# Optimization experiments

Measured on AMD Instinct MI355X. Metric: run time of the kernel, lower is better.

The kernel has to match this reference:

```python
import jax, jax.numpy as jnp
import numpy as np

N_FEAT = 1024
NEG_BIG = -1e30  # finite stand-in for -inf to avoid NaNs on fully-masked rows


def setup_inputs() -> dict:
    key = jax.random.key(0)
    k1, k2, k3 = jax.random.split(key, 3)
    T, C = 4096, 1024
    x = jax.random.normal(k1, (T, C), dtype=jnp.float32)
    W = jax.random.normal(k2, (C, 3 * N_FEAT), dtype=jnp.float32) * 0.02
    b = jax.random.normal(k3, (3 * N_FEAT,), dtype=jnp.float32) * 0.02
    return {"x": x, "W": W, "b": b, "n_padd": 256}


def reference(x, W, b, n_padd):
    T, C = x.shape
    qkv = x @ W + b  # [T, 3*N_FEAT]
    q, k, v = jnp.split(qkv, 3, axis=1)  # each [T, N_FEAT]
    att = (q @ k.T) * (1.0 / jnp.sqrt(jnp.float32(N_FEAT)))  # [T, T]
    idx = jnp.arange(T)
    causal = idx[None, :] <= idx[:, None]
    data = (idx[None, :] >= n_padd) & (idx[:, None] >= n_padd)
    mask = causal & data
    att = jnp.where(mask, att, NEG_BIG)
    p = jax.nn.softmax(att, axis=-1)  # fully-masked rows -> uniform, zeroed below
    y = p @ v  # [T, N_FEAT]
    # kernel only stores rows >= n_padd; padded rows defined as zero here
    y = jnp.where(idx[:, None] >= n_padd, y, 0.0)
    return y
```

## Files before the change

### kernel.cpp

```cpp
#include <hip/hip_runtime.h>
#include <hip/hip_bf16.h>
#include <stdint.h>
#include <stddef.h>

#define TT 4096
#define CC 1024
#define NFD 1024
#define N3 3072
#define PB0 1152
#define PB2 2176

typedef __bf16 bf16;
typedef __bf16 bf16x8 __attribute__((ext_vector_type(8)));
typedef __bf16 bf16x4 __attribute__((ext_vector_type(4)));
typedef float f32x4 __attribute__((ext_vector_type(4)));

typedef const __attribute__((address_space(1))) unsigned char gl_u8;
typedef __attribute__((address_space(3))) unsigned char lds_u8;

__device__ __forceinline__ void glds16(const void* g, void* l) {
  __builtin_amdgcn_global_load_lds((gl_u8*)g, (lds_u8*)l, 16, 0, 0);
}

__device__ __forceinline__ void stage128x32(const bf16* __restrict__ src, int ld, bf16* lds, int tid) {
  const int lane = tid & 63;
  const int w = tid >> 6;
#pragma unroll
  for (int p = 0; p < 2; ++p) {
    const int lbyte = w * 2048 + p * 1024;
    const int row = (lbyte >> 6) + (lane >> 2);
    const int kel = (lane & 3) << 3;
    glds16(src + row * ld + kel, (char*)lds + lbyte);
  }
}

__device__ __forceinline__ void gemm_core(const bf16* __restrict__ A, const bf16* __restrict__ B,
                                          int lda, int ldb, int ksteps,
                                          bf16* As, bf16* Bs, int tid, f32x4 (&acc)[4][4]) {
  const int lane = tid & 63;
  const int w = tid >> 6;
  const int wm = (w >> 1) * 64;
  const int wn = (w & 1) * 64;
  const int lrow = lane & 15;
  const int lko = (lane >> 4) * 8;
  stage128x32(A, lda, As, tid);
  stage128x32(B, ldb, Bs, tid);
  __syncthreads();
  for (int ks = 0; ks < ksteps; ++ks) {
    const bf16* Ac = As + (ks & 1) * 4096;
    const bf16* Bc = Bs + (ks & 1) * 4096;
    if (ks + 1 < ksteps) {
      stage128x32(A + (ks + 1) * 32, lda, As + ((ks + 1) & 1) * 4096, tid);
      stage128x32(B + (ks + 1) * 32, ldb, Bs + ((ks + 1) & 1) * 4096, tid);
    }
    bf16x8 af[4], bfr[4];
#pragma unroll
    for (int i = 0; i < 4; ++i)
      af[i] = *(const bf16x8*)(Ac + (wm + i * 16 + lrow) * 32 + lko);
#pragma unroll
    for (int i = 0; i < 4; ++i)
      bfr[i] = *(const bf16x8*)(Bc + (wn + i * 16 + lrow) * 32 + lko);
#pragma unroll
    for (int mi = 0; mi < 4; ++mi)
#pragma unroll
      for (int ni = 0; ni < 4; ++ni)
        acc[mi][ni] = __builtin_amdgcn_mfma_f32_16x16x32_bf16(af[mi], bfr[ni], acc[mi][ni], 0, 0, 0);
    __syncthreads();
  }
}

__global__ __launch_bounds__(256) void k_prep(const float* __restrict__ x, bf16* __restrict__ xb,
                                              const float* __restrict__ Wsrc, bf16* __restrict__ WbT,
                                              float* __restrict__ l) {
  __shared__ float Ls[64][68];
  const int tid = threadIdx.x;
  if (blockIdx.x < 2048) {
    int idx = (blockIdx.x * 256 + tid) * 8;
    f32x4 a = *(const f32x4*)(x + idx);
    f32x4 b = *(const f32x4*)(x + idx + 4);
    bf16x8 o;
#pragma unroll
    for (int j = 0; j < 4; ++j) { o[j] = (bf16)a[j]; o[4 + j] = (bf16)b[j]; }
    *(bf16x8*)(xb + idx) = o;
    return;
  }
  if (blockIdx.x == 2048 + 768) {
    f32x4 z = (f32x4){0.f, 0.f, 0.f, 0.f};
#pragma unroll
    for (int qq = 0; qq < 4; ++qq)
      *(f32x4*)(l + (qq * 256 + tid) * 4) = z;
    return;
  }
  const int bid = blockIdx.x - 2048;
  const int n0 = (bid % 48) * 64;
  const int c0 = (bid / 48) * 64;
#pragma unroll
  for (int qq = 0; qq < 4; ++qq) {
    int lin = qq * 1024 + tid * 4;
    int r = lin >> 6, cc = lin & 63;
    f32x4 v = *(const f32x4*)(Wsrc + (size_t)(c0 + r) * N3 + n0 + cc);
#pragma unroll
    for (int j = 0; j < 4; ++j) Ls[r][cc + j] = v[j];
  }
  __syncthreads();
#pragma unroll
  for (int qq = 0; qq < 4; ++qq) {
    int lin = qq * 1024 + tid * 4;
    int nr = lin >> 6, cc = lin & 63;
    bf16x4 o;
#pragma unroll
    for (int j = 0; j < 4; ++j) o[j] = (bf16)Ls[cc + j][nr];
    *(bf16x4*)(WbT + (size_t)(n0 + nr) * CC + c0 + cc) = o;
  }
}

__global__ __launch_bounds__(256, 2) void k_qkv(const bf16* __restrict__ xb, const bf16* __restrict__ wbt,
                                                const float* __restrict__ bias,
                                                bf16* __restrict__ q, bf16* __restrict__ k,
                                                bf16* __restrict__ vT) {
  __shared__ bf16 As[2 * 128 * 32], Bs[2 * 128 * 32];
  const int tid = threadIdx.x;
  const int id = blockIdx.x;
  const int r = id & 7;
  const int s = id >> 3;
  const int it = 4 * r + (s & 3);
  const int jt = s >> 2;
  const int m0 = it * 128;
  const int n0 = jt * 128;
  f32x4 acc[4][4];
#pragma unroll
  for (int i = 0; i < 4; ++i)
#pragma unroll
    for (int j = 0; j < 4; ++j) acc[i][j] = (f32x4){0.f, 0.f, 0.f, 0.f};

  gemm_core(xb + (size_t)m0 * CC, wbt + (size_t)n0 * CC, CC, CC, CC / 32, As, Bs, tid, acc);

  const int lane = tid & 63;
  const int w = tid >> 6;
  const int wm = (w >> 1) * 64, wn = (w & 1) * 64;
  const int seg = n0 >> 10;
#pragma unroll
  for (int mi = 0; mi < 4; ++mi) {
    const int tB = m0 + wm + mi * 16 + ((lane >> 4) << 2);
#pragma unroll
    for (int ni = 0; ni < 4; ++ni) {
      const int n = n0 + wn + ni * 16 + (lane & 15);
      const float bb = bias[n];
      f32x4 a = acc[mi][ni];
      if (seg == 2) {
        bf16x4 pv;
#pragma unroll
        for (int r2 = 0; r2 < 4; ++r2) pv[r2] = (bf16)(a[r2] + bb);
        *(bf16x4*)(vT + (size_t)(n - 2048) * TT + tB) = pv;
      } else {
        bf16* dst = (seg == 0) ? q : k;
        const int nl = n & 1023;
#pragma unroll
        for (int r2 = 0; r2 < 4; ++r2) dst[(size_t)(tB + r2) * NFD + nl] = (bf16)(a[r2] + bb);
      }
    }
  }
}

__global__ __launch_bounds__(256, 2) void k_scores(const bf16* __restrict__ q, const bf16* __restrict__ kk,
                                                   bf16* __restrict__ P, float* __restrict__ l,
                                                   const int* __restrict__ npadd_p) {
  const int id = blockIdx.x;
  const int lin = (id & 7) * 66 + (id >> 3);
  int band, rem;
  if (lin < 228)      { band = 0; rem = lin; }
  else if (lin < 392) { band = 1; rem = lin - 228; }
  else if (lin < 492) { band = 2; rem = lin - 392; }
  else                { band = 3; rem = lin - 492; }
  int it, jt;
  if (rem < 28) {
    int itp = (int)((sqrtf(8.0f * (float)rem + 1.0f) - 1.0f) * 0.5f);
    while ((itp + 1) * (itp + 2) / 2 <= rem) ++itp;
    while (itp * (itp + 1) / 2 > rem) --itp;
    it = band * 8 + itp;
    jt = band * 8 + (rem - itp * (itp + 1) / 2);
  } else {
    const int rem2 = rem - 28;
    it = band * 8 + 7 + (rem2 >> 3);
    jt = band * 8 + (rem2 & 7);
  }
  const int np = *npadd_p;
  const int jt0 = np >> 7;
  if (jt < jt0) return;

  __shared__ bf16 As[2 * 128 * 32], Bs[2 * 128 * 32];
  const int tid = threadIdx.x;
  f32x4 acc[4][4];
#pragma unroll
  for (int i = 0; i < 4; ++i)
#pragma unroll
    for (int j = 0; j < 4; ++j) acc[i][j] = (f32x4){0.f, 0.f, 0.f, 0.f};

  gemm_core(q + (size_t)it * 128 * CC, kk + (size_t)jt * 128 * CC, CC, CC, CC / 32, As, Bs, tid, acc);

  const int lane = tid & 63;
  const int w = tid >> 6;
  const int wm = (w >> 1) * 64, wn = (w & 1) * 64;
  const float scale = 0.03125f;
#pragma unroll
  for (int mi = 0; mi < 4; ++mi) {
    const int iB = it * 128 + wm + mi * 16 + ((lane >> 4) << 2);
    float rs[4] = {0.f, 0.f, 0.f, 0.f};
#pragma unroll
    for (int ni = 0; ni < 4; ++ni) {
      const int j = jt * 128 + wn + ni * 16 + (lane & 15);
      f32x4 a = acc[mi][ni];
#pragma unroll
      for (int r = 0; r < 4; ++r) {
        const int i = iB + r;
        float p = 0.f;
        if (j <= i && j >= np && i >= np) p = __expf(a[r] * scale);
        const bf16 pb = (bf16)p;
        P[(size_t)i * TT + j] = pb;
        rs[r] += (float)pb;
      }
    }
#pragma unroll
    for (int r = 0; r < 4; ++r) {
      float v = rs[r];
      v += __shfl_xor(v, 1);
      v += __shfl_xor(v, 2);
      v += __shfl_xor(v, 4);
      v += __shfl_xor(v, 8);
      if ((lane & 15) == 0) atomicAdd(&l[iB + r], v);
    }
  }
}

__global__ __launch_bounds__(256, 2) void k_pvc(const bf16* __restrict__ P, const bf16* __restrict__ vT,
                                                bf16* __restrict__ part0, bf16* __restrict__ part1,
                                                bf16* __restrict__ part2,
                                                const float* __restrict__ l, float* __restrict__ y,
                                                const int* __restrict__ npadd_p) {
  const int id = blockIdx.x;
  const int kgrp = id >> 3;
  const int d0 = (kgrp & 7) * 128;
  const int p = (id & 7) + 8 * (kgrp >> 3);
  const int it = p >> 2;
  const int c = p & 3;
  const int np = *npadd_p;
  const int jt0 = np >> 7;
  const int lo = (c == 0) ? 0 : (c == 1 ? 9 : (c == 2 ? 17 : 25));
  const int hi = (c == 0) ? 9 : (c == 1 ? 17 : (c == 2 ? 25 : 32));
  const int jlo = max(lo, jt0);
  const int jhi = min(hi, it + 1);
  if (jlo >= jhi) return;

  __shared__ bf16 As[2 * 128 * 32], Bs[2 * 128 * 32];
  const int tid = threadIdx.x;
  f32x4 acc[4][4];
#pragma unroll
  for (int i = 0; i < 4; ++i)
#pragma unroll
    for (int j = 0; j < 4; ++j) acc[i][j] = (f32x4){0.f, 0.f, 0.f, 0.f};

  gemm_core(P + (size_t)it * 128 * TT + (size_t)jlo * 128,
            vT + (size_t)d0 * TT + (size_t)jlo * 128,
            TT, TT, (jhi - jlo) * 4, As, Bs, tid, acc);

  const int lane = tid & 63;
  const int w = tid >> 6;
  const int wm = (w >> 1) * 64, wn = (w & 1) * 64;
  const bool sole = (jlo == jt0) && (jhi == it + 1);
  if (sole) {
#pragma unroll
    for (int mi = 0; mi < 4; ++mi) {
      const int iB = it * 128 + wm + mi * 16 + ((lane >> 4) << 2);
      float inv4[4];
#pragma unroll
      for (int r = 0; r < 4; ++r) {
        const int i = iB + r;
        inv4[r] = (i >= np) ? (1.0f / l[i]) : 0.0f;
      }
#pragma unroll
      for (int ni = 0; ni < 4; ++ni) {
        const int d = d0 + wn + ni * 16 + (lane & 15);
        f32x4 a = acc[mi][ni];
#pragma unroll
        for (int r = 0; r < 4; ++r)
          y[(size_t)(iB + r) * NFD + d] = a[r] * inv4[r];
      }
    }
  } else if (c == 3) {
#pragma unroll
    for (int mi = 0; mi < 4; ++mi) {
      const int iB = it * 128 + wm + mi * 16 + ((lane >> 4) << 2);
#pragma unroll
      for (int ni = 0; ni < 4; ++ni) {
        const int d = d0 + wn + ni * 16 + (lane & 15);
        f32x4 a = acc[mi][ni];
#pragma unroll
        for (int r = 0; r < 4; ++r)
          y[(size_t)(iB + r) * NFD + d] = a[r];
      }
    }
  } else {
    bf16* __restrict__ part = (c == 0) ? part0 : (c == 1 ? part1 : part2);
    const int base = (c == 2) ? (PB2 * NFD) : (PB0 * NFD);
#pragma unroll
    for (int mi = 0; mi < 4; ++mi) {
      const int iB = it * 128 + wm + mi * 16 + ((lane >> 4) << 2);
#pragma unroll
      for (int ni = 0; ni < 4; ++ni) {
        const int d = d0 + wn + ni * 16 + (lane & 15);
        f32x4 a = acc[mi][ni];
#pragma unroll
        for (int r = 0; r < 4; ++r)
          part[(size_t)(iB + r) * NFD + d - base] = (bf16)a[r];
      }
    }
  }
}

__global__ __launch_bounds__(256) void k_norm(const bf16* __restrict__ part0, const bf16* __restrict__ part1,
                                              const bf16* __restrict__ part2,
                                              const float* __restrict__ l, float* __restrict__ y,
                                              const int* __restrict__ npadd_p) {
  const int idx = (blockIdx.x * 256 + threadIdx.x) * 8;
  const int i = idx >> 10;
  const int np = *npadd_p;
  if (i < np) {
    f32x4 z = (f32x4){0.f, 0.f, 0.f, 0.f};
    *(f32x4*)(y + idx) = z;
    *(f32x4*)(y + idx + 4) = z;
    return;
  }
  const int jt0 = np >> 7;
  const int it = i >> 7;
  const int ip1 = it + 1;
  const bool a0 = (max(0, jt0)  < min(9, ip1));
  const bool a1 = (max(9, jt0)  < min(17, ip1));
  const bool a2 = (max(17, jt0) < min(25, ip1));
  const bool a3 = (max(25, jt0) < min(32, ip1));
  const int cnt = (int)a0 + (int)a1 + (int)a2 + (int)a3;
  if (cnt <= 1) return;
  float s[8] = {0.f, 0.f, 0.f, 0.f, 0.f, 0.f, 0.f, 0.f};
  if (a0) {
    bf16x8 a = *(const bf16x8*)(part0 + idx - PB0 * NFD);
#pragma unroll
    for (int j = 0; j < 8; ++j) s[j] += (float)a[j];
  }
  if (a1) {
    bf16x8 a = *(const bf16x8*)(part1 + idx - PB0 * NFD);
#pragma unroll
    for (int j = 0; j < 8; ++j) s[j] += (float)a[j];
  }
  if (a2) {
    bf16x8 a = *(const bf16x8*)(part2 + idx - PB2 * NFD);
#pragma unroll
    for (int j = 0; j < 8; ++j) s[j] += (float)a[j];
  }
  if (a3) {
    f32x4 a = *(const f32x4*)(y + idx);
    f32x4 b = *(const f32x4*)(y + idx + 4);
#pragma unroll
    for (int j = 0; j < 4; ++j) { s[j] += a[j]; s[4 + j] += b[j]; }
  }
  const float inv = 1.0f / l[i];
  f32x4 o0, o1;
#pragma unroll
  for (int j = 0; j < 4; ++j) { o0[j] = s[j] * inv; o1[j] = s[4 + j] * inv; }
  *(f32x4*)(y + idx) = o0;
  *(f32x4*)(y + idx + 4) = o1;
}

extern "C" void kernel_launch(void* const* d_in, const int* in_sizes, int n_in,
                              void* d_out, int out_size, void* d_ws, size_t ws_size,
                              hipStream_t stream) {
  const float* x = (const float*)d_in[0];
  const float* W = (const float*)d_in[1];
  const float* b = (const float*)d_in[2];
  const int* npadd = (const int*)d_in[3];
  float* y = (float*)d_out;

  char* ws = (char*)d_ws;
  const size_t MB = 1u << 20;
  bf16* q  = (bf16*)(ws + 0 * MB);
  bf16* kk = (bf16*)(ws + 8 * MB);
  bf16* part0 = (bf16*)(ws + 0 * MB);
  bf16* part1 = (bf16*)(ws + (size_t)(TT - PB0) * NFD * 2);
  bf16* part2 = (bf16*)(ws + (size_t)2 * (TT - PB0) * NFD * 2);
  bf16* vT = (bf16*)(ws + 16 * MB);
  float* l = (float*)(ws + 24 * MB);
  bf16* P  = (bf16*)(ws + 24 * MB + 65536);
  bf16* xb = P;
  bf16* WbT = (bf16*)((char*)P + 8 * MB);

  k_prep<<<dim3(2048 + 768 + 1), 256, 0, stream>>>(x, xb, W, WbT, l);
  k_qkv<<<dim3(768), 256, 0, stream>>>(xb, WbT, b, q, kk, vT);
  k_scores<<<dim3(528), 256, 0, stream>>>(q, kk, P, l, npadd);
  k_pvc<<<dim3(1024), 256, 0, stream>>>(P, vT, part0, part1, part2, l, y, npadd);
  k_norm<<<dim3((TT * NFD) / (256 * 8)), 256, 0, stream>>>(part0, part1, part2, l, y, npadd);
}
```

Before: 118.2 us.

## Use 4-stage LDS ring with explicit vmcnt waits in QK^T GEMM

Replaces the double-buffered GEMM core in the attention-score kernel with a four-buffer ring that prefetches three k-steps ahead. It waits on vmcnt counts and raw s_barrier instead of the __syncthreads after each step. The aim is to hide global-to-LDS load latency behind MFMA work. The cost is a doubled LDS footprint (64KB per block), which may reduce occupancy, and a hand-counted vmcnt that depends on stage128x32 issuing exactly four loads per thread per call.

Result: slower. 132.9 us (+12.4%).

```diff
diff --git a/kernel.cpp b/kernel.cpp
--- a/kernel.cpp
+++ b/kernel.cpp
@@ -66,6 +66,56 @@
       for (int ni = 0; ni < 4; ++ni)
         acc[mi][ni] = __builtin_amdgcn_mfma_f32_16x16x32_bf16(af[mi], bfr[ni], acc[mi][ni], 0, 0, 0);
     __syncthreads();
+  }
+}
+
+__device__ __forceinline__ void gemm_core_p3(const bf16* __restrict__ A, const bf16* __restrict__ B,
+                                             int lda, int ldb, int ksteps,
+                                             bf16* As, bf16* Bs, int tid, f32x4 (&acc)[4][4]) {
+  const int lane = tid & 63;
+  const int w = tid >> 6;
+  const int wm = (w >> 1) * 64;
+  const int wn = (w & 1) * 64;
+  const int lrow = lane & 15;
+  const int lko = (lane >> 4) * 8;
+  stage128x32(A, lda, As, tid);
+  stage128x32(B, ldb, Bs, tid);
+  stage128x32(A + 32, lda, As + 4096, tid);
+  stage128x32(B + 32, ldb, Bs + 4096, tid);
+  stage128x32(A + 64, lda, As + 8192, tid);
+  stage128x32(B + 64, ldb, Bs + 8192, tid);
+  int cur = 0, nxt = 3;
+  for (int ks = 0; ks < ksteps; ++ks) {
+    if (ks + 3 < ksteps) {
+      stage128x32(A + (size_t)(ks + 3) * 32, lda, As + nxt * 4096, tid);
+      stage128x32(B + (size_t)(ks + 3) * 32, ldb, Bs + nxt * 4096, tid);
+      asm volatile("s_waitcnt vmcnt(12)" ::: "memory");
+    } else if (ks + 2 < ksteps) {
+      asm volatile("s_waitcnt vmcnt(8)" ::: "memory");
+    } else if (ks + 1 < ksteps) {
+      asm volatile("s_waitcnt vmcnt(4)" ::: "memory");
+    } else {
+      asm volatile("s_waitcnt vmcnt(0)" ::: "memory");
+    }
+    __builtin_amdgcn_s_barrier();
+    __builtin_amdgcn_sched_barrier(0);
+    const bf16* Ac = As + cur * 4096;
+    const bf16* Bc = Bs + cur * 4096;
+    bf16x8 af[4], bfr[4];
+#pragma unroll
+    for (int i = 0; i < 4; ++i)
+      af[i] = *(const bf16x8*)(Ac + (wm + i * 16 + lrow) * 32 + lko);
+#pragma unroll
+    for (int i = 0; i < 4; ++i)
+      bfr[i] = *(const bf16x8*)(Bc + (wn + i * 16 + lrow) * 32 + lko);
+#pragma unroll
+    for (int mi = 0; mi < 4; ++mi)
+#pragma unroll
+      for (int ni = 0; ni < 4; ++ni)
+        acc[mi][ni] = __builtin_amdgcn_mfma_f32_16x16x32_bf16(af[mi], bfr[ni], acc[mi][ni], 0, 0, 0);
+    __builtin_amdgcn_s_barrier();
+    cur = (cur + 1) & 3;
+    nxt = (nxt + 1) & 3;
   }
 }
 
@@ -188,7 +238,7 @@
   const int jt0 = np >> 7;
   if (jt < jt0) return;
 
-  __shared__ bf16 As[2 * 128 * 32], Bs[2 * 128 * 32];
+  __shared__ bf16 As[4 * 128 * 32], Bs[4 * 128 * 32];
   const int tid = threadIdx.x;
   f32x4 acc[4][4];
 #pragma unroll
@@ -196,7 +246,7 @@
 #pragma unroll
     for (int j = 0; j < 4; ++j) acc[i][j] = (f32x4){0.f, 0.f, 0.f, 0.f};
 
-  gemm_core(q + (size_t)it * 128 * CC, kk + (size_t)jt * 128 * CC, CC, CC, CC / 32, As, Bs, tid, acc);
+  gemm_core_p3(q + (size_t)it * 128 * CC, kk + (size_t)jt * 128 * CC, CC, CC, CC / 32, As, Bs, tid, acc);
 
   const int lane = tid & 63;
   const int w = tid >> 6;
```
